# Performance work log

Measured on AMD Instinct MI355X. Metric: run time of the kernel, lower is better.

## Reference

```python
import jax, jax.numpy as jnp
import numpy as np

N_NODES = 10000
N_REL = 40
N_BASES = 30
HIDDEN = 100
N_EDGES = 320000


def setup_inputs() -> dict:
    key = jax.random.key(0)
    ks = jax.random.split(key, 11)
    s = 0.05  # param init scale
    inp = {
        "comp1": jax.random.normal(ks[0], (N_REL, N_BASES), jnp.float32) * s,
        "basis1": jax.random.normal(ks[1], (N_BASES, N_NODES, HIDDEN), jnp.float32) * s,
        "root1": jax.random.normal(ks[2], (N_NODES, HIDDEN), jnp.float32) * s,
        "bias1": jax.random.normal(ks[3], (HIDDEN,), jnp.float32) * s,
        "comp2": jax.random.normal(ks[4], (N_REL, N_BASES), jnp.float32) * s,
        "basis2": jax.random.normal(ks[5], (N_BASES, HIDDEN, HIDDEN), jnp.float32) * s,
        "root2": jax.random.normal(ks[6], (HIDDEN, HIDDEN), jnp.float32) * s,
        "bias2": jax.random.normal(ks[7], (HIDDEN,), jnp.float32) * s,
        "emb_rel": jax.random.normal(ks[8], (N_REL + 1, HIDDEN), jnp.float32) * s,
        "edge_index": jax.random.randint(ks[9], (2, N_EDGES), 0, N_NODES, jnp.int64),
        "edge_type": jax.random.randint(ks[10], (N_EDGES,), 0, N_REL, jnp.int64),
    }
    return inp


def _agg_mean_per_relation(msg, dst, rel, n_nodes, n_rel):
    # PyG RGCNConv loops over relations with aggr='mean': messages are
    # mean-aggregated per (target node, relation), then summed over relations.
    seg = dst * n_rel + rel  # combined (node, relation) segment id
    sums = jax.ops.segment_sum(msg, seg, num_segments=n_nodes * n_rel)
    ones = jnp.ones((msg.shape[0], 1), msg.dtype)
    cnt = jax.ops.segment_sum(ones, seg, num_segments=n_nodes * n_rel)
    mean = sums / jnp.maximum(cnt, 1.0)
    return mean.reshape(n_nodes, n_rel, -1).sum(axis=1)  # [N, hidden]


def reference(comp1, basis1, root1, bias1, comp2, basis2, root2, bias2,
              emb_rel, edge_index, edge_type):
    src, dst = edge_index[0], edge_index[1]
    n_nodes = root1.shape[0]
    n_rel = comp1.shape[0]

    # ---- conv1 (x = None -> featureless: weight acts as embedding over node ids)
    # basis decomposition: W1[r] = sum_b comp1[r,b] * basis1[b]
    W1 = jnp.einsum('rb,bno->rno', comp1, basis1)  # [R, N, H]
    msg1 = W1[edge_type, src]                       # per-edge gather [E, H]
    agg1 = _agg_mean_per_relation(msg1, dst, edge_type, n_nodes, n_rel)
    # root term with x=None is root1[arange(N)] = root1 itself
    h = jax.nn.relu(agg1 + root1 + bias1)           # [N, H]

    # ---- conv2 (dense node features)
    W2 = jnp.einsum('rb,bdo->rdo', comp2, basis2)   # [R, H, H]
    Hx = jnp.einsum('nd,rdo->rno', h, W2)           # all-relation transforms [R, N, H]
    msg2 = Hx[edge_type, src]                       # [E, H]
    agg2 = _agg_mean_per_relation(msg2, dst, edge_type, n_nodes, n_rel)
    x = agg2 + h @ root2 + bias2                    # [N, H]

    # ---- relation embedding lookup (padding_idx=0 -> row 0 is zero)
    emb = emb_rel.at[0].set(0.0)
    rel_embedded = emb[edge_type]                   # [E, H]
    return (x, rel_embedded)
```

## Files before the change

### kernel.cpp

```cpp
#include <hip/hip_runtime.h>
#include <hip/hip_bf16.h>
#include <cstdint>
#include <cstddef>

#define E_EDGES 320000
#define NN 10000
#define NRELS 40
#define NB 30
#define HID 100
#define NHTOT (NN*HID)
#define R2 41
#define KTOT 4224
#define NROWS_PAD 10048
#define SPLITK 4
#define KB_PER 33
#define RSPLIT 2
#define RPB (NRELS/RSPLIT)

typedef short bf16x8 __attribute__((ext_vector_type(8)));
typedef float f32x4 __attribute__((ext_vector_type(4)));

__device__ inline ushort f2bf(float f) {
  uint x = __float_as_uint(f);
  return (ushort)((x + 0x7fffu + ((x >> 16) & 1u)) >> 16);
}
__device__ inline float bflo(uint u) { return __uint_as_float(u << 16); }
__device__ inline float bfhi(uint u) { return __uint_as_float(u & 0xffff0000u); }

__device__ inline void gload16(const void* g, void* l) {
  __builtin_amdgcn_global_load_lds(
      (const __attribute__((address_space(1))) void*)g,
      (__attribute__((address_space(3))) void*)l, 16, 0, 0);
}

__global__ void k_count(const int* __restrict__ dst, const int* __restrict__ et,
                        int* __restrict__ cnt_nr, int* __restrict__ deg) {
  int e = blockIdx.x * blockDim.x + threadIdx.x;
  if (e >= E_EDGES) return;
  int d = dst[e], r = et[e];
  atomicAdd(&cnt_nr[d * NRELS + r], 1);
  atomicAdd(&deg[d], 1);
}

__global__ void k_scan(const int* __restrict__ deg, int* __restrict__ rowptr) {
  __shared__ int ssum[256];
  int t = threadIdx.x;
  const int per = (NN + 255) / 256;
  int base = t * per;
  int s = 0;
  for (int k = 0; k < per; ++k) { int i = base + k; if (i < NN) s += deg[i]; }
  ssum[t] = s; __syncthreads();
  for (int off = 1; off < 256; off <<= 1) {
    int v = (t >= off) ? ssum[t - off] : 0;
    __syncthreads();
    ssum[t] += v;
    __syncthreads();
  }
  int pre = (t == 0) ? 0 : ssum[t - 1];
  for (int k = 0; k < per; ++k) {
    int i = base + k;
    if (i < NN) { rowptr[i] = pre; pre += deg[i]; }
  }
  if (t == 255) rowptr[NN] = ssum[255];
}

__global__ void k_bucket(const int* __restrict__ src, const int* __restrict__ dst,
                         const int* __restrict__ et, const int* __restrict__ rowptr,
                         int* __restrict__ fill, int* __restrict__ ebuf) {
  int e = blockIdx.x * blockDim.x + threadIdx.x;
  if (e >= E_EDGES) return;
  int d = dst[e];
  int pos = rowptr[d] + atomicAdd(&fill[d], 1);
  ebuf[pos] = (src[e] << 6) | et[e];
}

__global__ __launch_bounds__(256) void k_w1b(const float* __restrict__ comp1,
                                             const float* __restrict__ basis1,
                                             uint* __restrict__ W1bf) {
  __shared__ float sct[NB][RPB];
  int t = threadIdx.x;
  int rbase = blockIdx.y * RPB;
  for (int i = t; i < RPB * NB; i += 256) {
    int r = i / NB, b = i - r * NB;
    sct[b][r] = comp1[(rbase + r) * NB + b];
  }
  __syncthreads();
  int i2 = blockIdx.x * 256 + t;
  if (i2 >= NHTOT / 2) return;
  float ax[RPB], ay[RPB];
#pragma unroll
  for (int r = 0; r < RPB; ++r) { ax[r] = 0.f; ay[r] = 0.f; }
  for (int b = 0; b < NB; ++b) {
    float2 v = ((const float2*)basis1)[(size_t)b * (NHTOT / 2) + i2];
#pragma unroll
    for (int r4 = 0; r4 < RPB / 4; ++r4) {
      float4 c = *(const float4*)&sct[b][r4 * 4];
      ax[r4*4+0] += c.x * v.x; ay[r4*4+0] += c.x * v.y;
      ax[r4*4+1] += c.y * v.x; ay[r4*4+1] += c.y * v.y;
      ax[r4*4+2] += c.z * v.x; ay[r4*4+2] += c.z * v.y;
      ax[r4*4+3] += c.w * v.x; ay[r4*4+3] += c.w * v.y;
    }
  }
#pragma unroll
  for (int r = 0; r < RPB; ++r)
    W1bf[(size_t)(rbase + r) * (NHTOT / 2) + i2] =
        (uint)f2bf(ax[r]) | ((uint)f2bf(ay[r]) << 16);
}

__global__ void k_w2(const float* __restrict__ comp2, const float* __restrict__ basis2,
                     float* __restrict__ W2f) {
  int i = blockIdx.x * 256 + threadIdx.x;
  if (i >= HID * HID) return;
  float v[NB];
#pragma unroll
  for (int b = 0; b < NB; ++b) v[b] = basis2[b * HID * HID + i];
  for (int r = 0; r < NRELS; ++r) {
    float a = 0.f;
#pragma unroll
    for (int b = 0; b < NB; ++b) a += comp2[r * NB + b] * v[b];
    W2f[r * HID * HID + i] = a;
  }
}

__global__ void k_bt(const float* __restrict__ W2f, const float* __restrict__ root2,
                     ushort* __restrict__ Bt) {
  int i = blockIdx.x * 256 + threadIdx.x;
  if (i >= 112 * KTOT) return;
  int col = i / KTOT, kk = i - col * KTOT;
  float v = 0.f;
  if (kk < R2 * HID && col < HID) {
    int r = kk / HID, k = kk - r * HID;
    v = (r < NRELS) ? W2f[(r * HID + k) * HID + col] : root2[k * HID + col];
  }
  Bt[i] = f2bf(v);
}

__global__ void k_agg1(const int* __restrict__ rowptr, const int* __restrict__ ebuf,
                       const int* __restrict__ cnt_nr, const uint* __restrict__ W1bf,
                       const float* __restrict__ root1, const float* __restrict__ bias1,
                       float* __restrict__ h) {
  int n = blockIdx.x, t = threadIdx.x;
  if (t >= 50) return;
  float a0 = 0.f, a1 = 0.f;
  int beg = rowptr[n], end = rowptr[n + 1];
  int j = beg;
  for (; j + 1 < end; j += 2) {
    int pk0 = ebuf[j], pk1 = ebuf[j + 1];
    int r0 = pk0 & 63, s0 = pk0 >> 6;
    int r1 = pk1 & 63, s1 = pk1 >> 6;
    float c0 = 1.0f / (float)cnt_nr[n * NRELS + r0];
    float c1 = 1.0f / (float)cnt_nr[n * NRELS + r1];
    uint u0 = W1bf[(size_t)(r0 * NN + s0) * 50 + t];
    uint u1 = W1bf[(size_t)(r1 * NN + s1) * 50 + t];
    a0 += c0 * bflo(u0) + c1 * bflo(u1);
    a1 += c0 * bfhi(u0) + c1 * bfhi(u1);
  }
  if (j < end) {
    int pk = ebuf[j];
    int r = pk & 63, s = pk >> 6;
    float c = 1.0f / (float)cnt_nr[n * NRELS + r];
    uint u = W1bf[(size_t)(r * NN + s) * 50 + t];
    a0 += c * bflo(u);
    a1 += c * bfhi(u);
  }
  int c0 = 2 * t, c1 = 2 * t + 1;
  float v0 = a0 + root1[n * HID + c0] + bias1[c0];
  float v1 = a1 + root1[n * HID + c1] + bias1[c1];
  h[n * HID + c0] = v0 > 0.f ? v0 : 0.f;
  h[n * HID + c1] = v1 > 0.f ? v1 : 0.f;
}

__global__ __launch_bounds__(128) void k_hbar(const int* __restrict__ rowptr,
                                              const int* __restrict__ ebuf,
                                              const int* __restrict__ cnt_nr,
                                              const float* __restrict__ h,
                                              uint* __restrict__ hbar) {
  __shared__ float acc[NRELS][HID];
  int n = blockIdx.x, t = threadIdx.x;
  for (int i = t; i < NRELS * HID; i += 128) ((float*)acc)[i] = 0.f;
  __syncthreads();
  if (t < HID) {
    int beg = rowptr[n], end = rowptr[n + 1];
    int j = beg;
    for (; j + 1 < end; j += 2) {
      int pk0 = ebuf[j], pk1 = ebuf[j + 1];
      int r0 = pk0 & 63, s0 = pk0 >> 6;
      int r1 = pk1 & 63, s1 = pk1 >> 6;
      float h0 = h[s0 * HID + t];
      float h1 = h[s1 * HID + t];
      acc[r0][t] += h0;
      acc[r1][t] += h1;
    }
    if (j < end) {
      int pk = ebuf[j];
      acc[pk & 63][t] += h[(pk >> 6) * HID + t];
    }
  }
  __syncthreads();
  uint* orow = hbar + (size_t)n * (KTOT / 2);
  for (int i = t; i < KTOT / 2; i += 128) {
    float v0 = 0.f, v1 = 0.f;
    if (i < R2 * 50) {
      int r = i / 50;
      int kk = (i - r * 50) * 2;
      if (r < NRELS) {
        int c = cnt_nr[n * NRELS + r];
        float coef = c ? 1.0f / (float)c : 0.f;
        v0 = acc[r][kk] * coef;
        v1 = acc[r][kk + 1] * coef;
      } else {
        v0 = h[n * HID + kk];
        v1 = h[n * HID + kk + 1];
      }
    }
    orow[i] = (uint)f2bf(v0) | ((uint)f2bf(v1) << 16);
  }
}

__global__ __launch_bounds__(256) void k_gemm(const ushort* __restrict__ hbar,
                                              const ushort* __restrict__ Bt,
                                              float* __restrict__ part) {
  __shared__ char lds[2][12288];
  int t = threadIdx.x;
  int wid = t >> 6, l = t & 63;
  int lrow = l & 15, g16 = l >> 4;
  int kb0 = blockIdx.y * KB_PER;
  int row0 = blockIdx.x * 64;

  f32x4 acc[7];
#pragma unroll
  for (int j = 0; j < 7; ++j) acc[j] = (f32x4){0.f, 0.f, 0.f, 0.f};

  auto stage = [&](int p, int buf) {
    int kbg = kb0 + p;
#pragma unroll
    for (int ci = 0; ci < 3; ++ci) {
      int qb = (wid * 3 + ci) * 64;
      int q = qb + l;
      const ushort* g;
      if (q < 448) {
        int col = q >> 2, c = q & 3;
        g = Bt + (size_t)col * KTOT + kbg * 32 + c * 8;
      } else if (q < 704) {
        int qq = q - 448;
        int row = qq >> 2, c = qq & 3;
        g = hbar + (size_t)(row0 + row) * KTOT + kbg * 32 + c * 8;
      } else {
        g = Bt;
      }
      gload16(g, &lds[buf][(size_t)qb * 16]);
    }
  };

  stage(0, 0);
  __syncthreads();

  int cur = 0;
  for (int p = 0; p < KB_PER; ++p) {
    if (p + 1 < KB_PER) stage(p + 1, cur ^ 1);
    const char* base = lds[cur];
    bf16x8 a = *(const bf16x8*)(base + 7168 + (wid * 16 + lrow) * 64 + g16 * 16);
#pragma unroll
    for (int j = 0; j < 7; ++j) {
      bf16x8 b = *(const bf16x8*)(base + (j * 16 + lrow) * 64 + g16 * 16);
      acc[j] = __builtin_amdgcn_mfma_f32_16x16x32_bf16(a, b, acc[j], 0, 0, 0);
    }
    __syncthreads();
    cur ^= 1;
  }

  float* pp = part + (size_t)blockIdx.y * NROWS_PAD * 112;
  int srow = row0 + wid * 16 + g16 * 4;
#pragma unroll
  for (int j = 0; j < 7; ++j) {
    int col = j * 16 + lrow;
#pragma unroll
    for (int v = 0; v < 4; ++v)
      pp[(size_t)(srow + v) * 112 + col] = acc[j][v];
  }
}

__global__ void k_red(const float* __restrict__ part, const float* __restrict__ bias2,
                      float* __restrict__ xout) {
  int i = blockIdx.x * 256 + threadIdx.x;
  if (i >= NHTOT) return;
  int n = i / HID, c = i - n * HID;
  float s = bias2[c];
#pragma unroll
  for (int g = 0; g < SPLITK; ++g)
    s += part[(size_t)g * NROWS_PAD * 112 + (size_t)n * 112 + c];
  xout[i] = s;
}

__global__ void k_emb(const float4* __restrict__ emb, const int* __restrict__ et,
                      float4* __restrict__ out2) {
  int i = blockIdx.x * 256 + threadIdx.x;
  if (i >= E_EDGES * 25) return;
  int e = i / 25, q = i - e * 25;
  int r = et[e];
  float4 v;
  if (r == 0) { v.x = 0.f; v.y = 0.f; v.z = 0.f; v.w = 0.f; }
  else v = emb[r * 25 + q];
  out2[i] = v;
}

extern "C" void kernel_launch(void* const* d_in, const int* in_sizes, int n_in,
                              void* d_out, int out_size, void* d_ws, size_t ws_size,
                              hipStream_t stream) {
  (void)in_sizes; (void)n_in; (void)out_size; (void)d_ws; (void)ws_size;

  const float* comp1  = (const float*)d_in[0];
  const float* basis1 = (const float*)d_in[1];
  const float* root1  = (const float*)d_in[2];
  const float* bias1  = (const float*)d_in[3];
  const float* comp2  = (const float*)d_in[4];
  const float* basis2 = (const float*)d_in[5];
  const float* root2  = (const float*)d_in[6];
  const float* bias2  = (const float*)d_in[7];
  const float* emb    = (const float*)d_in[8];
  const int*   ei     = (const int*)d_in[9];
  const int*   et     = (const int*)d_in[10];
  const int* srcp = ei;
  const int* dstp = ei + E_EDGES;

  float* xout = (float*)d_out;
  float* scratch = xout + NHTOT;
  int*   cnt_nr = (int*)scratch;
  int*   deg    = cnt_nr + 400000;
  int*   rowptr = deg + 10000;
  int*   fill   = rowptr + 10004;
  int*   ebuf   = fill + 10000;
  float* W2f    = scratch + 750016;
  ushort* Bt    = (ushort*)(scratch + 1150016);
  float* h      = scratch + 1386560;
  uint*  W1bf   = (uint*)(scratch + 2386560);
  uint*  hbar   = (uint*)(scratch + 2386560);
  float* part   = scratch + 23607936;

  hipMemsetAsync(cnt_nr, 0, (size_t)430004 * sizeof(int), stream);
  hipMemsetAsync((char*)hbar + (size_t)NN * KTOT * 2, 0,
                 (size_t)(NROWS_PAD - NN) * KTOT * 2, stream);

  k_count <<<(E_EDGES + 255) / 256, 256, 0, stream>>>(dstp, et, cnt_nr, deg);
  k_scan  <<<1, 256, 0, stream>>>(deg, rowptr);
  k_bucket<<<(E_EDGES + 255) / 256, 256, 0, stream>>>(srcp, dstp, et, rowptr, fill, ebuf);

  k_w2 <<<(HID * HID + 255) / 256, 256, 0, stream>>>(comp2, basis2, W2f);
  k_bt <<<(112 * KTOT + 255) / 256, 256, 0, stream>>>(W2f, root2, Bt);
  k_w1b<<<dim3((NHTOT / 2 + 255) / 256, RSPLIT), 256, 0, stream>>>(comp1, basis1, W1bf);

  k_agg1<<<NN, 64, 0, stream>>>(rowptr, ebuf, cnt_nr, W1bf, root1, bias1, h);
  k_hbar<<<NN, 128, 0, stream>>>(rowptr, ebuf, cnt_nr, h, hbar);
  k_gemm<<<dim3(NROWS_PAD / 64, SPLITK), 256, 0, stream>>>((const ushort*)hbar, Bt, part);
  k_red <<<(NHTOT + 255) / 256, 256, 0, stream>>>(part, bias2, xout);

  k_emb<<<(E_EDGES * 25 + 255) / 256, 256, 0, stream>>>((const float4*)emb, et,
                                                        (float4*)(xout + NHTOT));
}
```

Baseline: 308.3 us.

## Split per-node edge loops across thread groups in agg1 and hbar

k_agg1 now uses 256 threads per node, with 5 groups of 50 lanes each handling a strided share of the edges. The partial sums are reduced through shared memory. k_hbar now uses 512 threads, with 5 groups of 100 lanes accumulating into the per-relation LDS table via shared-memory atomics. Both changes aim to raise memory-level parallelism for the gather-heavy aggregation, since each node has about 32 edges. k_w1b switches to float2 vector math, likely to get packed FMA. The cost is LDS atomic contention, an extra sync, and idle lanes in the larger blocks.

```diff
diff --git a/kernel.cpp b/kernel.cpp
--- a/kernel.cpp
+++ b/kernel.cpp
@@ -19,6 +19,7 @@
 
 typedef short bf16x8 __attribute__((ext_vector_type(8)));
 typedef float f32x4 __attribute__((ext_vector_type(4)));
+typedef float f32x2 __attribute__((ext_vector_type(2)));
 
 __device__ inline ushort f2bf(float f) {
   uint x = __float_as_uint(f);
@@ -87,24 +88,24 @@
   __syncthreads();
   int i2 = blockIdx.x * 256 + t;
   if (i2 >= NHTOT / 2) return;
-  float ax[RPB], ay[RPB];
-#pragma unroll
-  for (int r = 0; r < RPB; ++r) { ax[r] = 0.f; ay[r] = 0.f; }
+  f32x2 acc[RPB];
+#pragma unroll
+  for (int r = 0; r < RPB; ++r) acc[r] = (f32x2){0.f, 0.f};
   for (int b = 0; b < NB; ++b) {
-    float2 v = ((const float2*)basis1)[(size_t)b * (NHTOT / 2) + i2];
+    f32x2 v = ((const f32x2*)basis1)[(size_t)b * (NHTOT / 2) + i2];
 #pragma unroll
     for (int r4 = 0; r4 < RPB / 4; ++r4) {
       float4 c = *(const float4*)&sct[b][r4 * 4];
-      ax[r4*4+0] += c.x * v.x; ay[r4*4+0] += c.x * v.y;
-      ax[r4*4+1] += c.y * v.x; ay[r4*4+1] += c.y * v.y;
-      ax[r4*4+2] += c.z * v.x; ay[r4*4+2] += c.z * v.y;
-      ax[r4*4+3] += c.w * v.x; ay[r4*4+3] += c.w * v.y;
+      acc[r4*4+0] += (f32x2){c.x, c.x} * v;
+      acc[r4*4+1] += (f32x2){c.y, c.y} * v;
+      acc[r4*4+2] += (f32x2){c.z, c.z} * v;
+      acc[r4*4+3] += (f32x2){c.w, c.w} * v;
     }
   }
 #pragma unroll
   for (int r = 0; r < RPB; ++r)
     W1bf[(size_t)(rbase + r) * (NHTOT / 2) + i2] =
-        (uint)f2bf(ax[r]) | ((uint)f2bf(ay[r]) << 16);
+        (uint)f2bf(acc[r].x) | ((uint)f2bf(acc[r].y) << 16);
 }
 
 __global__ void k_w2(const float* __restrict__ comp2, const float* __restrict__ basis2,
@@ -135,77 +136,69 @@
   Bt[i] = f2bf(v);
 }
 
-__global__ void k_agg1(const int* __restrict__ rowptr, const int* __restrict__ ebuf,
-                       const int* __restrict__ cnt_nr, const uint* __restrict__ W1bf,
-                       const float* __restrict__ root1, const float* __restrict__ bias1,
-                       float* __restrict__ h) {
+__global__ __launch_bounds__(256) void k_agg1(const int* __restrict__ rowptr,
+                                              const int* __restrict__ ebuf,
+                                              const int* __restrict__ cnt_nr,
+                                              const uint* __restrict__ W1bf,
+                                              const float* __restrict__ root1,
+                                              const float* __restrict__ bias1,
+                                              float* __restrict__ h) {
+  __shared__ float red[5][2][50];
   int n = blockIdx.x, t = threadIdx.x;
-  if (t >= 50) return;
-  float a0 = 0.f, a1 = 0.f;
-  int beg = rowptr[n], end = rowptr[n + 1];
-  int j = beg;
-  for (; j + 1 < end; j += 2) {
-    int pk0 = ebuf[j], pk1 = ebuf[j + 1];
-    int r0 = pk0 & 63, s0 = pk0 >> 6;
-    int r1 = pk1 & 63, s1 = pk1 >> 6;
-    float c0 = 1.0f / (float)cnt_nr[n * NRELS + r0];
-    float c1 = 1.0f / (float)cnt_nr[n * NRELS + r1];
-    uint u0 = W1bf[(size_t)(r0 * NN + s0) * 50 + t];
-    uint u1 = W1bf[(size_t)(r1 * NN + s1) * 50 + t];
-    a0 += c0 * bflo(u0) + c1 * bflo(u1);
-    a1 += c0 * bfhi(u0) + c1 * bfhi(u1);
-  }
-  if (j < end) {
-    int pk = ebuf[j];
-    int r = pk & 63, s = pk >> 6;
-    float c = 1.0f / (float)cnt_nr[n * NRELS + r];
-    uint u = W1bf[(size_t)(r * NN + s) * 50 + t];
-    a0 += c * bflo(u);
-    a1 += c * bfhi(u);
-  }
-  int c0 = 2 * t, c1 = 2 * t + 1;
-  float v0 = a0 + root1[n * HID + c0] + bias1[c0];
-  float v1 = a1 + root1[n * HID + c1] + bias1[c1];
-  h[n * HID + c0] = v0 > 0.f ? v0 : 0.f;
-  h[n * HID + c1] = v1 > 0.f ? v1 : 0.f;
-}
-
-__global__ __launch_bounds__(128) void k_hbar(const int* __restrict__ rowptr,
+  int g = t / 50, c = t - g * 50;
+  if (g < 5) {
+    float a0 = 0.f, a1 = 0.f;
+    int beg = rowptr[n], end = rowptr[n + 1];
+    for (int j = beg + g; j < end; j += 5) {
+      int pk = ebuf[j];
+      int r = pk & 63, s = pk >> 6;
+      float cf = 1.0f / (float)cnt_nr[n * NRELS + r];
+      uint u = W1bf[(size_t)(r * NN + s) * 50 + c];
+      a0 += cf * bflo(u);
+      a1 += cf * bfhi(u);
+    }
+    red[g][0][c] = a0;
+    red[g][1][c] = a1;
+  }
+  __syncthreads();
+  if (t < 50) {
+    float a0 = red[0][0][t] + red[1][0][t] + red[2][0][t] + red[3][0][t] + red[4][0][t];
+    float a1 = red[0][1][t] + red[1][1][t] + red[2][1][t] + red[3][1][t] + red[4][1][t];
+    int c0 = 2 * t, c1 = 2 * t + 1;
+    float v0 = a0 + root1[n * HID + c0] + bias1[c0];
+    float v1 = a1 + root1[n * HID + c1] + bias1[c1];
+    h[n * HID + c0] = v0 > 0.f ? v0 : 0.f;
+    h[n * HID + c1] = v1 > 0.f ? v1 : 0.f;
+  }
+}
+
+__global__ __launch_bounds__(512) void k_hbar(const int* __restrict__ rowptr,
                                               const int* __restrict__ ebuf,
                                               const int* __restrict__ cnt_nr,
                                               const float* __restrict__ h,
                                               uint* __restrict__ hbar) {
   __shared__ float acc[NRELS][HID];
   int n = blockIdx.x, t = threadIdx.x;
-  for (int i = t; i < NRELS * HID; i += 128) ((float*)acc)[i] = 0.f;
-  __syncthreads();
-  if (t < HID) {
+  for (int i = t; i < NRELS * HID; i += 512) ((float*)acc)[i] = 0.f;
+  __syncthreads();
+  int g = t / HID, c = t - g * HID;
+  if (g < 5) {
     int beg = rowptr[n], end = rowptr[n + 1];
-    int j = beg;
-    for (; j + 1 < end; j += 2) {
-      int pk0 = ebuf[j], pk1 = ebuf[j + 1];
-      int r0 = pk0 & 63, s0 = pk0 >> 6;
-      int r1 = pk1 & 63, s1 = pk1 >> 6;
-      float h0 = h[s0 * HID + t];
-      float h1 = h[s1 * HID + t];
-      acc[r0][t] += h0;
-      acc[r1][t] += h1;
-    }
-    if (j < end) {
+    for (int j = beg + g; j < end; j += 5) {
       int pk = ebuf[j];
-      acc[pk & 63][t] += h[(pk >> 6) * HID + t];
+      atomicAdd(&acc[pk & 63][c], h[(size_t)(pk >> 6) * HID + c]);
     }
   }
   __syncthreads();
   uint* orow = hbar + (size_t)n * (KTOT / 2);
-  for (int i = t; i < KTOT / 2; i += 128) {
+  for (int i = t; i < KTOT / 2; i += 512) {
     float v0 = 0.f, v1 = 0.f;
     if (i < R2 * 50) {
       int r = i / 50;
       int kk = (i - r * 50) * 2;
       if (r < NRELS) {
-        int c = cnt_nr[n * NRELS + r];
-        float coef = c ? 1.0f / (float)c : 0.f;
+        int cc = cnt_nr[n * NRELS + r];
+        float coef = cc ? 1.0f / (float)cc : 0.f;
         v0 = acc[r][kk] * coef;
         v1 = acc[r][kk + 1] * coef;
       } else {
@@ -349,8 +342,8 @@
   k_bt <<<(112 * KTOT + 255) / 256, 256, 0, stream>>>(W2f, root2, Bt);
   k_w1b<<<dim3((NHTOT / 2 + 255) / 256, RSPLIT), 256, 0, stream>>>(comp1, basis1, W1bf);
 
-  k_agg1<<<NN, 64, 0, stream>>>(rowptr, ebuf, cnt_nr, W1bf, root1, bias1, h);
-  k_hbar<<<NN, 128, 0, stream>>>(rowptr, ebuf, cnt_nr, h, hbar);
+  k_agg1<<<NN, 256, 0, stream>>>(rowptr, ebuf, cnt_nr, W1bf, root1, bias1, h);
+  k_hbar<<<NN, 512, 0, stream>>>(rowptr, ebuf, cnt_nr, h, hbar);
   k_gemm<<<dim3(NROWS_PAD / 64, SPLITK), 256, 0, stream>>>((const ushort*)hbar, Bt, part);
   k_red <<<(NHTOT + 255) / 256, 256, 0, stream>>>(part, bias2, xout);
 
```

Result: slower. 420.7 us (+36.4%).
